# Kernel optimization log

Measured on AMD Instinct MI355X. Metric: run time of the kernel, lower is better.

The kernel has to match this reference:

```python
import jax, jax.numpy as jnp
import numpy as np

VOCAB = 50000
EMB = 100
BATCH = 2048
CTX = 10


def setup_inputs() -> dict:
    key = jax.random.key(0)
    k1, k2, k3, k4 = jax.random.split(key, 4)
    x_positive = jax.random.randint(k1, (BATCH, CTX), 0, VOCAB)
    y = jax.random.randint(k2, (BATCH,), 0, VOCAB)
    emb_v = jax.random.normal(k3, (VOCAB, EMB), dtype=jnp.float32)
    emb_u = jax.random.normal(k4, (VOCAB, EMB), dtype=jnp.float32)
    return {"x_positive": x_positive, "y": y, "emb_v": emb_v, "emb_u": emb_u}


def reference(x_positive, y, emb_v, emb_u):
    # h: mean of context embeddings, [B, E]
    h = emb_v[x_positive].mean(axis=1)
    # positive score: dot(emb_u[y], h) per row -> -logsigmoid
    pos = -jax.nn.log_sigmoid(jnp.einsum("be,be->b", emb_u[y], h))
    # negative score: (-U) @ h for every vocab word -> sigmoid -> sum over vocab -> log
    neg_scores = -jnp.einsum("be,ve->bv", h, emb_u)  # [B, V]
    neg = jnp.log(jax.nn.sigmoid(neg_scores).sum(axis=1))
    return jnp.mean(pos + neg)
```

## Files before the change

kernel.cpp:

```cpp
#include <hip/hip_runtime.h>
#include <math.h>

#define VOCAB 50000
#define VPAD  50048
#define EMB   100
#define BATCH 2048
#define CTX   10

#define NVT   391
#define BC    8
#define PROWS (2 * NVT)
#define NMG   (VPAD / 16)
#define CVTB  (NMG / 4)
#define HBLK  (BATCH / 2)

#define LOG2E 1.44269504088896340736f

#if __has_builtin(__builtin_amdgcn_exp2f)
#define EXP2(x) __builtin_amdgcn_exp2f(x)
#else
#define EXP2(x) __expf((x) * 0.6931471805599453f)
#endif


typedef __attribute__((ext_vector_type(8))) int   i32x8;
typedef __attribute__((ext_vector_type(4))) float f32x4;

__global__ __launch_bounds__(256)
void k_prep(const float* __restrict__ u, unsigned char* __restrict__ ub8,
            const int* __restrict__ x, const float* __restrict__ emb_v,
            float* __restrict__ hf, unsigned char* __restrict__ hb8,
            float* __restrict__ out) {
    const int blk = blockIdx.x;
    const int t   = threadIdx.x;
    if (blk < CVTB) {
        const int mgid = blk * 4 + (t >> 6);
        const int L    = t & 63;
        const int c16  = L & 15;
        const int q    = L >> 4;
        const int row  = mgid * 16 + c16;
        const int e0   = q * 32;
        i32x8 o = (i32x8)0;
        if (row < VOCAB) {
            if (q < 3) {
                const float4* p = (const float4*)&u[row * EMB + e0];
#pragma unroll
                for (int j = 0; j < 8; ++j) {
                    const float4 v = p[j];
                    int wd = __builtin_amdgcn_cvt_pk_fp8_f32(v.x * LOG2E, v.y * LOG2E, 0, false);
                    wd     = __builtin_amdgcn_cvt_pk_fp8_f32(v.z * LOG2E, v.w * LOG2E, wd, true);
                    o[j] = wd;
                }
            } else {
                const float4 v = *(const float4*)&u[row * EMB + 96];
                int wd = __builtin_amdgcn_cvt_pk_fp8_f32(v.x * LOG2E, v.y * LOG2E, 0, false);
                wd     = __builtin_amdgcn_cvt_pk_fp8_f32(v.z * LOG2E, v.w * LOG2E, wd, true);
                o[0] = wd;
            }
        }
        *(i32x8*)&ub8[((size_t)mgid * 64 + L) * 32] = o;
    } else {
        const int b = (blk - CVTB) * 2 + (t >> 7);
        const int e = t & 127;
        if (blk == CVTB && t == 0) out[0] = 0.0f;
        float s = 0.0f;
        if (e < EMB) {
#pragma unroll
            for (int c = 0; c < CTX; ++c) {
                const int idx = x[b * CTX + c];
                s += emb_v[idx * EMB + e];
            }
            s *= (1.0f / CTX);
            hf[b * EMB + e] = s;
        }
        const unsigned char f8 =
            (unsigned char)(__builtin_amdgcn_cvt_pk_fp8_f32(s, 0.0f, 0, false) & 0xFF);
        hb8[((b >> 4) * 64 + (e >> 5) * 16 + (b & 15)) * 32 + (e & 31)] = f8;
    }
}

__global__ __launch_bounds__(256, 4)
void k_neg(const unsigned char* __restrict__ hb8, const unsigned char* __restrict__ ub8,
           float* __restrict__ partial) {
    const int t   = threadIdx.x;
    const int w   = t >> 6;
    const int L   = t & 63;
    const int wvh = w & 1;
    const int wbh = w >> 1;
    const int vy  = blockIdx.y;

    i32x8 af[4];
#pragma unroll
    for (int mi = 0; mi < 4; ++mi)
        af[mi] = *(const i32x8*)&ub8[(((size_t)vy * 8 + wvh * 4 + mi) * 64 + L) * 32];

    const int b0base = blockIdx.x * (BATCH / BC);
    const int prow   = (2 * vy + wvh) * BATCH;
    const int NT     = (BATCH / BC) / 64;

    i32x8 bf[2];
#pragma unroll
    for (int ni = 0; ni < 2; ++ni)
        bf[ni] = *(const i32x8*)&hb8[((size_t)((b0base >> 4) + wbh * 2 + ni) * 64 + L) * 32];

#pragma unroll 1
    for (int bt = 0; bt < NT; ++bt) {
        const int b0 = b0base + bt * 64;

        f32x4 acc[4][2];
#pragma unroll
        for (int mi = 0; mi < 4; ++mi)
#pragma unroll
            for (int ni = 0; ni < 2; ++ni) acc[mi][ni] = (f32x4)(0.0f);

#pragma unroll
        for (int mi = 0; mi < 4; ++mi)
#pragma unroll
            for (int ni = 0; ni < 2; ++ni)
                acc[mi][ni] = __builtin_amdgcn_mfma_scale_f32_16x16x128_f8f6f4(
                    af[mi], bf[ni], acc[mi][ni],
                    0, 0,
                    0, 0x7F7F7F7F,
                    0, 0x7F7F7F7F);

        const int btn = (bt + 1 < NT) ? bt + 1 : bt;
        const int Bgn = (b0base + btn * 64) >> 4;
#pragma unroll
        for (int ni = 0; ni < 2; ++ni)
            bf[ni] = *(const i32x8*)&hb8[((size_t)(Bgn + wbh * 2 + ni) * 64 + L) * 32];

#pragma unroll
        for (int ni = 0; ni < 2; ++ni) {
            float p = 0.0f;
#pragma unroll
            for (int mi = 0; mi < 4; ++mi) {
                const float ea = EXP2(acc[mi][ni][0]);
                const float eb = EXP2(acc[mi][ni][1]);
                const float ec = EXP2(acc[mi][ni][2]);
                const float ed = EXP2(acc[mi][ni][3]);
                const float n1 = 2.0f + ea + eb;
                const float d1 = fmaf(ea, eb, n1 - 1.0f);
                const float n2 = 2.0f + ec + ed;
                const float d2 = fmaf(ec, ed, n2 - 1.0f);
                const float N  = fmaf(n1, d2, n2 * d1);
                p = fmaf(N, __builtin_amdgcn_rcpf(d1 * d2), p);
            }
            p += __shfl_down(p, 32);
            p += __shfl_down(p, 16);
            if (L < 16)
                partial[prow + b0 + wbh * 32 + ni * 16 + L] = p;
        }
    }
}

__global__ void k_redfinal(const int* __restrict__ y, const float* __restrict__ hf,
                           const float* __restrict__ u, const float* __restrict__ partial,
                           float* __restrict__ out) {
    const int t    = threadIdx.x;
    const int lane = t & 63;
    const int w    = t >> 6;
    const int b    = blockIdx.x * 64 + lane;
    float s = 0.0f;
    for (int r = w; r < PROWS; r += 16)
        s += partial[r * BATCH + b];
    __shared__ float red[16][64];
    red[w][lane] = s;
    __syncthreads();
    if (w == 0) {
        float ns = -(float)(VPAD - VOCAB) * 0.5f;
#pragma unroll
        for (int i = 0; i < 16; ++i) ns += red[i][lane];

        const int yi = y[b];
        const float4* hp = (const float4*)&hf[b * EMB];
        const float4* up = (const float4*)&u[yi * EMB];
        float dot = 0.0f;
#pragma unroll
        for (int qq = 0; qq < EMB / 4; ++qq) {
            const float4 a = hp[qq];
            const float4 c = up[qq];
            dot += a.x * c.x + a.y * c.y + a.z * c.z + a.w * c.w;
        }
        const float pos = fmaxf(-dot, 0.0f) + log1pf(__expf(-fabsf(dot)));
        float val = pos + logf(ns);
#pragma unroll
        for (int off = 32; off; off >>= 1) val += __shfl_down(val, off, 64);
        if (lane == 0) atomicAdd(out, val * (1.0f / BATCH));
    }
}

extern "C" void kernel_launch(void* const* d_in, const int* in_sizes, int n_in,
                              void* d_out, int out_size, void* d_ws, size_t ws_size,
                              hipStream_t stream) {
    const int*   x     = (const int*)d_in[0];
    const int*   y     = (const int*)d_in[1];
    const float* emb_v = (const float*)d_in[2];
    const float* emb_u = (const float*)d_in[3];
    float* out = (float*)d_out;

    float*         hf      = (float*)d_ws;
    float*         partial = hf + BATCH * EMB;
    unsigned char* hb8     = (unsigned char*)(partial + PROWS * BATCH);
    unsigned char* ub8     = hb8 + (size_t)(BATCH / 16) * 2048;

    k_prep    <<<dim3(CVTB + HBLK), dim3(256), 0, stream>>>(emb_u, ub8, x, emb_v, hf, hb8, out);
    k_neg     <<<dim3(BC, NVT), dim3(256), 0, stream>>>(hb8, ub8, partial);
    k_redfinal<<<dim3(BATCH / 64), dim3(1024), 0, stream>>>(y, hf, emb_u, partial, out);
}
```

Baseline: 128.9 us.

## Replace partial-sum buffer with atomic accumulation and re-split k_neg waves

k_neg no longer writes a 782-row partial-sum array that a separate reduction pass must read. Each wave now atomically adds its per-batch sums straight into a 2048-float neg_sum buffer, which k_prep zeroes. Each wave now covers 2 vocab tiles and all 32 batch columns per iteration, and the occupancy hint rises from 4 to 6. The final kernel becomes a simple per-batch pass, at the cost of many contended float atomics on a small buffer and the loss of B-fragment prefetch.

```diff
diff --git a/kernel.cpp b/kernel.cpp
--- a/kernel.cpp
+++ b/kernel.cpp
@@ -9,7 +9,6 @@
 
 #define NVT   391
 #define BC    8
-#define PROWS (2 * NVT)
 #define NMG   (VPAD / 16)
 #define CVTB  (NMG / 4)
 #define HBLK  (BATCH / 2)
@@ -30,7 +29,7 @@
 void k_prep(const float* __restrict__ u, unsigned char* __restrict__ ub8,
             const int* __restrict__ x, const float* __restrict__ emb_v,
             float* __restrict__ hf, unsigned char* __restrict__ hb8,
-            float* __restrict__ out) {
+            float* __restrict__ neg_sum, float* __restrict__ out) {
     const int blk = blockIdx.x;
     const int t   = threadIdx.x;
     if (blk < CVTB) {
@@ -60,9 +59,11 @@
         }
         *(i32x8*)&ub8[((size_t)mgid * 64 + L) * 32] = o;
     } else {
-        const int b = (blk - CVTB) * 2 + (t >> 7);
+        const int hb = blk - CVTB;
+        if (hb < 8) neg_sum[hb * 256 + t] = 0.0f;
+        if (hb == 0 && t == 0) out[0] = 0.0f;
+        const int b = hb * 2 + (t >> 7);
         const int e = t & 127;
-        if (blk == CVTB && t == 0) out[0] = 0.0f;
         float s = 0.0f;
         if (e < EMB) {
 #pragma unroll
@@ -79,42 +80,39 @@
     }
 }
 
-__global__ __launch_bounds__(256, 4)
+__global__ __launch_bounds__(256, 6)
 void k_neg(const unsigned char* __restrict__ hb8, const unsigned char* __restrict__ ub8,
-           float* __restrict__ partial) {
-    const int t   = threadIdx.x;
-    const int w   = t >> 6;
-    const int L   = t & 63;
-    const int wvh = w & 1;
-    const int wbh = w >> 1;
-    const int vy  = blockIdx.y;
+           float* __restrict__ neg_sum) {
+    const int t  = threadIdx.x;
+    const int w  = t >> 6;
+    const int L  = t & 63;
+    const int vy = blockIdx.y;
 
-    i32x8 af[4];
+    i32x8 af[2];
 #pragma unroll
-    for (int mi = 0; mi < 4; ++mi)
-        af[mi] = *(const i32x8*)&ub8[(((size_t)vy * 8 + wvh * 4 + mi) * 64 + L) * 32];
+    for (int mi = 0; mi < 2; ++mi)
+        af[mi] = *(const i32x8*)&ub8[(((size_t)vy * 8 + w * 2 + mi) * 64 + L) * 32];
 
     const int b0base = blockIdx.x * (BATCH / BC);
-    const int prow   = (2 * vy + wvh) * BATCH;
-    const int NT     = (BATCH / BC) / 64;
-
-    i32x8 bf[2];
-#pragma unroll
-    for (int ni = 0; ni < 2; ++ni)
-        bf[ni] = *(const i32x8*)&hb8[((size_t)((b0base >> 4) + wbh * 2 + ni) * 64 + L) * 32];
 
 #pragma unroll 1
-    for (int bt = 0; bt < NT; ++bt) {
-        const int b0 = b0base + bt * 64;
+    for (int bt = 0; bt < 8; ++bt) {
+        const int b0  = b0base + bt * 32;
+        const int Bg0 = b0 >> 4;
 
-        f32x4 acc[4][2];
+        i32x8 bf[2];
 #pragma unroll
-        for (int mi = 0; mi < 4; ++mi)
+        for (int ni = 0; ni < 2; ++ni)
+            bf[ni] = *(const i32x8*)&hb8[((size_t)(Bg0 + ni) * 64 + L) * 32];
+
+        f32x4 acc[2][2];
+#pragma unroll
+        for (int mi = 0; mi < 2; ++mi)
 #pragma unroll
             for (int ni = 0; ni < 2; ++ni) acc[mi][ni] = (f32x4)(0.0f);
 
 #pragma unroll
-        for (int mi = 0; mi < 4; ++mi)
+        for (int mi = 0; mi < 2; ++mi)
 #pragma unroll
             for (int ni = 0; ni < 2; ++ni)
                 acc[mi][ni] = __builtin_amdgcn_mfma_scale_f32_16x16x128_f8f6f4(
@@ -123,17 +121,11 @@
                     0, 0x7F7F7F7F,
                     0, 0x7F7F7F7F);
 
-        const int btn = (bt + 1 < NT) ? bt + 1 : bt;
-        const int Bgn = (b0base + btn * 64) >> 4;
-#pragma unroll
-        for (int ni = 0; ni < 2; ++ni)
-            bf[ni] = *(const i32x8*)&hb8[((size_t)(Bgn + wbh * 2 + ni) * 64 + L) * 32];
-
 #pragma unroll
         for (int ni = 0; ni < 2; ++ni) {
             float p = 0.0f;
 #pragma unroll
-            for (int mi = 0; mi < 4; ++mi) {
+            for (int mi = 0; mi < 2; ++mi) {
                 const float ea = EXP2(acc[mi][ni][0]);
                 const float eb = EXP2(acc[mi][ni][1]);
                 const float ec = EXP2(acc[mi][ni][2]);
@@ -148,45 +140,32 @@
             p += __shfl_down(p, 32);
             p += __shfl_down(p, 16);
             if (L < 16)
-                partial[prow + b0 + wbh * 32 + ni * 16 + L] = p;
+                atomicAdd(&neg_sum[b0 + ni * 16 + L], p);
         }
     }
 }
 
-__global__ void k_redfinal(const int* __restrict__ y, const float* __restrict__ hf,
-                           const float* __restrict__ u, const float* __restrict__ partial,
-                           float* __restrict__ out) {
-    const int t    = threadIdx.x;
-    const int lane = t & 63;
-    const int w    = t >> 6;
-    const int b    = blockIdx.x * 64 + lane;
-    float s = 0.0f;
-    for (int r = w; r < PROWS; r += 16)
-        s += partial[r * BATCH + b];
-    __shared__ float red[16][64];
-    red[w][lane] = s;
-    __syncthreads();
-    if (w == 0) {
-        float ns = -(float)(VPAD - VOCAB) * 0.5f;
+__global__ void k_final(const int* __restrict__ y, const float* __restrict__ hf,
+                        const float* __restrict__ u, const float* __restrict__ neg_sum,
+                        float* __restrict__ out) {
+    const int b = blockIdx.x * 256 + threadIdx.x;
+    const float ns = neg_sum[b] - (float)(VPAD - VOCAB) * 0.5f;
+
+    const int yi = y[b];
+    const float4* hp = (const float4*)&hf[b * EMB];
+    const float4* up = (const float4*)&u[yi * EMB];
+    float dot = 0.0f;
 #pragma unroll
-        for (int i = 0; i < 16; ++i) ns += red[i][lane];
-
-        const int yi = y[b];
-        const float4* hp = (const float4*)&hf[b * EMB];
-        const float4* up = (const float4*)&u[yi * EMB];
-        float dot = 0.0f;
+    for (int qq = 0; qq < EMB / 4; ++qq) {
+        const float4 a = hp[qq];
+        const float4 c = up[qq];
+        dot += a.x * c.x + a.y * c.y + a.z * c.z + a.w * c.w;
+    }
+    const float pos = fmaxf(-dot, 0.0f) + log1pf(__expf(-fabsf(dot)));
+    float val = pos + logf(ns);
 #pragma unroll
-        for (int qq = 0; qq < EMB / 4; ++qq) {
-            const float4 a = hp[qq];
-            const float4 c = up[qq];
-            dot += a.x * c.x + a.y * c.y + a.z * c.z + a.w * c.w;
-        }
-        const float pos = fmaxf(-dot, 0.0f) + log1pf(__expf(-fabsf(dot)));
-        float val = pos + logf(ns);
-#pragma unroll
-        for (int off = 32; off; off >>= 1) val += __shfl_down(val, off, 64);
-        if (lane == 0) atomicAdd(out, val * (1.0f / BATCH));
-    }
+    for (int off = 32; off; off >>= 1) val += __shfl_down(val, off, 64);
+    if ((threadIdx.x & 63) == 0) atomicAdd(out, val * (1.0f / BATCH));
 }
 
 extern "C" void kernel_launch(void* const* d_in, const int* in_sizes, int n_in,
@@ -199,11 +178,11 @@
     float* out = (float*)d_out;
 
     float*         hf      = (float*)d_ws;
-    float*         partial = hf + BATCH * EMB;
-    unsigned char* hb8     = (unsigned char*)(partial + PROWS * BATCH);
+    float*         neg_sum = hf + BATCH * EMB;
+    unsigned char* hb8     = (unsigned char*)(neg_sum + BATCH);
     unsigned char* ub8     = hb8 + (size_t)(BATCH / 16) * 2048;
 
-    k_prep    <<<dim3(CVTB + HBLK), dim3(256), 0, stream>>>(emb_u, ub8, x, emb_v, hf, hb8, out);
-    k_neg     <<<dim3(BC, NVT), dim3(256), 0, stream>>>(hb8, ub8, partial);
-    k_redfinal<<<dim3(BATCH / 64), dim3(1024), 0, stream>>>(y, hf, emb_u, partial, out);
+    k_prep <<<dim3(CVTB + HBLK), dim3(256), 0, stream>>>(emb_u, ub8, x, emb_v, hf, hb8, neg_sum, out);
+    k_neg  <<<dim3(BC, NVT), dim3(256), 0, stream>>>(hb8, ub8, neg_sum);
+    k_final<<<dim3(BATCH / 256), dim3(256), 0, stream>>>(y, hf, emb_u, neg_sum, out);
 }
```

Measured after the change: 195.3 us. 51.5% more time.
